# Performance work log

Hardware: AMD Instinct MI355X
Metric: run time of the kernel (lower is better)

## Reference

```python
import jax, jax.numpy as jnp
import numpy as np
import math

B, T, D, H = 4, 2048, 1024, 16
DH = D // H


def setup_inputs() -> dict:
    key = jax.random.key(0)
    k1, k2, k3 = jax.random.split(key, 3)
    x = jax.random.normal(k1, (B, T, D), dtype=jnp.float32)
    # causal mask: True = masked (positions j > i)
    attn_mask = jnp.triu(jnp.ones((T, T), dtype=bool), k=1)
    key_padding_mask = jnp.zeros((B, T), dtype=bool)  # no padding
    W_qkv = jax.random.normal(k2, (D, 3 * D), dtype=jnp.float32) / math.sqrt(D)
    W_out = jax.random.normal(k3, (D, D), dtype=jnp.float32) / math.sqrt(D)
    return {"x": x, "W_qkv": W_qkv, "W_out": W_out,
            "attn_mask": attn_mask, "key_padding_mask": key_padding_mask}


def reference(x, W_qkv, W_out, attn_mask, key_padding_mask):
    # qkv projection (bias=False)
    qkv = x @ W_qkv                                   # [B,T,3D]
    q, k, v = jnp.split(qkv, 3, axis=-1)              # each [B,T,D]
    # reshape to heads: [B,H,T,DH]
    q = q.reshape(B, T, H, DH).transpose(0, 2, 1, 3)
    k = k.reshape(B, T, H, DH).transpose(0, 2, 1, 3)
    v = v.reshape(B, T, H, DH).transpose(0, 2, 1, 3)
    scale = 1.0 / math.sqrt(DH)
    scores = jnp.einsum('bhqd,bhkd->bhqk', q, k) * scale   # [B,H,T,T]
    neg_inf = jnp.float32(-jnp.inf)
    scores = jnp.where(attn_mask[None, None, :, :], neg_inf, scores)
    scores = jnp.where(key_padding_mask[:, None, None, :], neg_inf, scores)
    attn = jax.nn.softmax(scores, axis=-1)            # dropout p=0.0 -> identity
    out = jnp.einsum('bhqk,bhkd->bhqd', attn, v)      # [B,H,T,DH]
    out = out.transpose(0, 2, 1, 3).reshape(B, T, D)
    return out @ W_out
```

## Files before the change

### kernel.cpp

```cpp
#include <hip/hip_runtime.h>
#include <hip/hip_bf16.h>

#define Bsz 4
#define T 2048
#define D 1024
#define H 16
#define DH 64

typedef unsigned short u16;
typedef __attribute__((ext_vector_type(8))) __bf16 bf16x8;
typedef __attribute__((ext_vector_type(4))) float f32x4;

__device__ inline u16 f2bf(float f) {
  union { float f; unsigned u; } v; v.f = f;
  unsigned r = (v.u + 0x7FFFu + ((v.u >> 16) & 1u)) >> 16;
  return (u16)r;
}
__device__ inline unsigned pack_bf16(float a, float b) {
  union { float f; unsigned u; } A, B; A.f = a; B.f = b;
  unsigned au = A.u + 0x8000u, bu = B.u + 0x8000u;
  return __builtin_amdgcn_perm(bu, au, 0x07060302);
}

__device__ inline void gll16(const u16* g, u16* l) {
  __builtin_amdgcn_global_load_lds((const __attribute__((address_space(1))) void*)g,
                                   (__attribute__((address_space(3))) void*)l, 16, 0, 0);
}

__global__ __launch_bounds__(256) void convert_f32_bf16(const float* __restrict__ in,
                                                        u16* __restrict__ out, int n4) {
  int i = blockIdx.x * 256 + threadIdx.x;
  if (i < n4) {
    float4 v = reinterpret_cast<const float4*>(in)[i];
    ushort4 o;
    o.x = f2bf(v.x); o.y = f2bf(v.y); o.z = f2bf(v.z); o.w = f2bf(v.w);
    reinterpret_cast<ushort4*>(out)[i] = o;
  }
}

__global__ __launch_bounds__(256) void transpose_f32_bf16(const float* __restrict__ in,
                                                          u16* __restrict__ out, int K, int N) {
  __shared__ float tile[32][33];
  int tx = threadIdx.x & 31, ty = threadIdx.x >> 5;
  int n0 = blockIdx.x * 32, k0 = blockIdx.y * 32;
  #pragma unroll
  for (int i = 0; i < 4; ++i)
    tile[ty + i * 8][tx] = in[(size_t)(k0 + ty + i * 8) * N + n0 + tx];
  __syncthreads();
  #pragma unroll
  for (int i = 0; i < 4; ++i)
    out[(size_t)(n0 + ty + i * 8) * K + k0 + tx] = f2bf(tile[tx][ty + i * 8]);
}

template <int MODE>
__global__ __launch_bounds__(256) void gemm128(const u16* __restrict__ A, const u16* __restrict__ BT,
                                               float* __restrict__ C,
                                               u16* __restrict__ Qh, u16* __restrict__ Kh,
                                               u16* __restrict__ VTh, int M, int N, int K) {
  __shared__ u16 As[128][32];
  __shared__ u16 Bs[128][32];
  int tid = threadIdx.x;
  int m0 = blockIdx.y * 128, n0 = blockIdx.x * 128;
  int w = tid >> 6, lane = tid & 63;
  int llo = lane & 15, lhi = lane >> 4;
  int wm = (w >> 1) * 64, wn = (w & 1) * 64;

  f32x4 acc[4][4];
  #pragma unroll
  for (int i = 0; i < 4; ++i)
    #pragma unroll
    for (int j = 0; j < 4; ++j) acc[i][j] = (f32x4){0.f, 0.f, 0.f, 0.f};

  const u16* gA = A + (size_t)(m0 + w * 32 + (lane >> 2)) * K + (lane & 3) * 8;
  const u16* gB = BT + (size_t)(n0 + w * 32 + (lane >> 2)) * K + (lane & 3) * 8;

  for (int k0 = 0; k0 < K; k0 += 32) {
    gll16(gA + k0, &As[w * 32][0]);
    gll16(gA + (size_t)16 * K + k0, &As[w * 32 + 16][0]);
    gll16(gB + k0, &Bs[w * 32][0]);
    gll16(gB + (size_t)16 * K + k0, &Bs[w * 32 + 16][0]);
    __syncthreads();
    bf16x8 af[4], bfr[4];
    #pragma unroll
    for (int i = 0; i < 4; ++i)
      af[i] = *reinterpret_cast<const bf16x8*>(&As[wm + i * 16 + llo][lhi * 8]);
    #pragma unroll
    for (int j = 0; j < 4; ++j)
      bfr[j] = *reinterpret_cast<const bf16x8*>(&Bs[wn + j * 16 + llo][lhi * 8]);
    #pragma unroll
    for (int i = 0; i < 4; ++i)
      #pragma unroll
      for (int j = 0; j < 4; ++j)
        acc[i][j] = __builtin_amdgcn_mfma_f32_16x16x32_bf16(af[i], bfr[j], acc[i][j], 0, 0, 0);
    __syncthreads();
  }

  if (MODE == 0) {
    #pragma unroll
    for (int i = 0; i < 4; ++i)
      #pragma unroll
      for (int j = 0; j < 4; ++j) {
        int nl = n0 + wn + j * 16 + llo;
        #pragma unroll
        for (int r = 0; r < 4; ++r) {
          int ml = m0 + wm + i * 16 + lhi * 4 + r;
          C[(size_t)ml * N + nl] = acc[i][j][r];
        }
      }
  } else {
    int seg = n0 >> 10;
    #pragma unroll
    for (int i = 0; i < 4; ++i) {
      int mbase = m0 + wm + i * 16 + lhi * 4;
      int t0 = mbase & (T - 1);
      int b_ = mbase >> 11;
      #pragma unroll
      for (int j = 0; j < 4; ++j) {
        int nl = n0 + wn + j * 16 + llo;
        int h = (nl >> 6) & 15, d = nl & 63;
        int bh = b_ * H + h;
        if (seg == 0) {
          #pragma unroll
          for (int r = 0; r < 4; ++r)
            Qh[((size_t)bh * T + t0 + r) * DH + d] = f2bf(acc[i][j][r] * 0.125f);
        } else if (seg == 1) {
          #pragma unroll
          for (int r = 0; r < 4; ++r)
            Kh[((size_t)bh * T + t0 + r) * DH + d] = f2bf(acc[i][j][r]);
        } else {
          uint2 p;
          p.x = pack_bf16(acc[i][j][0], acc[i][j][1]);
          p.y = pack_bf16(acc[i][j][2], acc[i][j][3]);
          *reinterpret_cast<uint2*>(&VTh[((size_t)bh * DH + d) * T + t0]) = p;
        }
      }
    }
  }
}

__global__ __launch_bounds__(1024, 4) void attn_fwd(const u16* __restrict__ Qh, const u16* __restrict__ Kh,
                                                    const u16* __restrict__ VTh, u16* __restrict__ AO) {
  __shared__ u16 QP[16][16][72];
  __shared__ u16 Ks[64][72];
  __shared__ u16 Vs[64][72];
  int tid = threadIdx.x;
  int qp = blockIdx.x, bh = blockIdx.y;
  int w = tid >> 6, lane = tid & 63;
  int llo = lane & 15, lhi = lane >> 4;

  int qrow_s = tid >> 2, qc = tid & 3;
  int krow_s = tid >> 4, kc = tid & 15;
  const u16* kbase = Kh + ((size_t)bh * T + krow_s) * DH + kc * 4;
  const u16* vbase = VTh + ((size_t)bh * DH + krow_s) * T + kc * 4;
  int b = bh >> 4, h = bh & 15;

  #pragma unroll 1
  for (int half = 0; half < 2; ++half) {
    int qt = half ? (7 - qp) : qp;
    int q0 = qt * 256;

    bf16x8 aq[2];
    {
      const uint4* g = reinterpret_cast<const uint4*>(
          Qh + ((size_t)bh * T + q0 + qrow_s) * DH + qc * 16);
      uint4 a = g[0], bb = g[1];
      uint4* dst = reinterpret_cast<uint4*>(&QP[w][qrow_s & 15][qc * 16]);
      dst[0] = a; dst[1] = bb;
      #pragma unroll
      for (int ks = 0; ks < 2; ++ks)
        aq[ks] = *reinterpret_cast<const bf16x8*>(&QP[w][llo][ks * 32 + lhi * 8]);
    }

    f32x4 o[4];
    #pragma unroll
    for (int i = 0; i < 4; ++i) o[i] = (f32x4){0.f, 0.f, 0.f, 0.f};
    float l_run = 0.f;

    int nj = 4 * qt + 4;
    uint2 ka = *reinterpret_cast<const uint2*>(kbase);
    uint2 va = *reinterpret_cast<const uint2*>(vbase);

    #pragma unroll 1
    for (int j = 0; j < nj; ++j) {
      __syncthreads();
      *reinterpret_cast<uint2*>(&Ks[krow_s][kc * 4]) = ka;
      *reinterpret_cast<uint2*>(&Vs[krow_s][kc * 4]) = va;
      if (j + 1 < nj) {
        ka = *reinterpret_cast<const uint2*>(kbase + (size_t)(j + 1) * 64 * DH);
        va = *reinterpret_cast<const uint2*>(vbase + (j + 1) * 64);
      } else if (half == 0) {
        ka = *reinterpret_cast<const uint2*>(kbase);
        va = *reinterpret_cast<const uint2*>(vbase);
      }
      __syncthreads();

      if (q0 + w * 16 + 15 >= j * 64) {
        f32x4 sc[4];
        #pragma unroll
        for (int kt = 0; kt < 4; ++kt) {
          bf16x8 bk0 = *reinterpret_cast<const bf16x8*>(&Ks[kt * 16 + llo][lhi * 8]);
          bf16x8 bk1 = *reinterpret_cast<const bf16x8*>(&Ks[kt * 16 + llo][32 + lhi * 8]);
          f32x4 z = (f32x4){0.f, 0.f, 0.f, 0.f};
          f32x4 t0 = __builtin_amdgcn_mfma_f32_16x16x32_bf16(bk0, aq[0], z, 0, 0, 0);
          sc[kt] = __builtin_amdgcn_mfma_f32_16x16x32_bf16(bk1, aq[1], t0, 0, 0, 0);
        }

        if (j >= 4 * qt) {
          int qrow_g = q0 + w * 16 + llo;
          #pragma unroll
          for (int kt = 0; kt < 4; ++kt)
            #pragma unroll
            for (int r = 0; r < 4; ++r) {
              int key_g = j * 64 + kt * 16 + lhi * 4 + r;
              if (key_g > qrow_g) sc[kt][r] = -__builtin_inff();
            }
        }

        float s_sum = 0.f;
        #pragma unroll
        for (int kt = 0; kt < 4; ++kt)
          #pragma unroll
          for (int r = 0; r < 4; ++r) {
            float p = __expf(sc[kt][r]);
            sc[kt][r] = p;
            s_sum += p;
          }
        s_sum += __shfl_xor(s_sum, 16);
        s_sum += __shfl_xor(s_sum, 32);
        l_run += s_sum;

        #pragma unroll
        for (int kt = 0; kt < 4; ++kt) {
          uint2 p;
          p.x = pack_bf16(sc[kt][0], sc[kt][1]);
          p.y = pack_bf16(sc[kt][2], sc[kt][3]);
          *reinterpret_cast<uint2*>(&QP[w][llo][kt * 16 + lhi * 4]) = p;
        }

        #pragma unroll
        for (int kk2 = 0; kk2 < 2; ++kk2) {
          bf16x8 pa = *reinterpret_cast<const bf16x8*>(&QP[w][llo][kk2 * 32 + lhi * 8]);
          #pragma unroll
          for (int nt = 0; nt < 4; ++nt) {
            bf16x8 bv = *reinterpret_cast<const bf16x8*>(&Vs[nt * 16 + llo][kk2 * 32 + lhi * 8]);
            o[nt] = __builtin_amdgcn_mfma_f32_16x16x32_bf16(pa, bv, o[nt], 0, 0, 0);
          }
        }
      }
    }

    #pragma unroll
    for (int r = 0; r < 4; ++r) {
      float inv = 1.f / __shfl(l_run, lhi * 4 + r);
      int t = q0 + w * 16 + lhi * 4 + r;
      #pragma unroll
      for (int nt = 0; nt < 4; ++nt)
        AO[((size_t)(b * T + t)) * D + h * 64 + nt * 16 + llo] = f2bf(o[nt][r] * inv);
    }
  }
}

extern "C" void kernel_launch(void* const* d_in, const int* in_sizes, int n_in,
                              void* d_out, int out_size, void* d_ws, size_t ws_size,
                              hipStream_t stream) {
  (void)in_sizes; (void)n_in; (void)out_size;
  const float* x = (const float*)d_in[0];
  const float* Wqkv = (const float*)d_in[1];
  const float* Wout = (const float*)d_in[2];
  float* out = (float*)d_out;

  char* ws = (char*)d_ws;
  size_t off = 0;
  u16* xb = (u16*)(ws + off);    off += (size_t)Bsz * T * D * 2;
  u16* WqkvT = (u16*)(ws + off); off += (size_t)3 * D * D * 2;
  u16* WoutT = (u16*)(ws + off); off += (size_t)D * D * 2;
  u16* Qh = (u16*)(ws + off);    off += (size_t)Bsz * H * T * DH * 2;
  u16* Kh = (u16*)(ws + off);    off += (size_t)Bsz * H * T * DH * 2;
  u16* VTh = (u16*)(ws + off);   off += (size_t)Bsz * H * DH * T * 2;
  u16* AO = xb;
  if (ws_size < off) return;

  int n4 = Bsz * T * D / 4;
  convert_f32_bf16<<<(n4 + 255) / 256, 256, 0, stream>>>(x, xb, n4);
  transpose_f32_bf16<<<dim3(3 * D / 32, D / 32), 256, 0, stream>>>(Wqkv, WqkvT, D, 3 * D);
  transpose_f32_bf16<<<dim3(D / 32, D / 32), 256, 0, stream>>>(Wout, WoutT, D, D);
  gemm128<1><<<dim3(3 * D / 128, Bsz * T / 128), 256, 0, stream>>>(xb, WqkvT, nullptr, Qh, Kh, VTh,
                                                                   Bsz * T, 3 * D, D);
  attn_fwd<<<dim3(4, Bsz * H), 1024, 0, stream>>>(Qh, Kh, VTh, AO);
  gemm128<0><<<dim3(D / 128, Bsz * T / 128), 256, 0, stream>>>(AO, WoutT, out, nullptr, nullptr, nullptr,
                                                               Bsz * T, D, D);
}
```

Measured before the change: 281.7 us.

## Replace QKV GEMM with 256x256 tiled, 4-stage pipelined kernel

```diff
diff --git a/kernel.cpp b/kernel.cpp
--- a/kernel.cpp
+++ b/kernel.cpp
@@ -50,6 +50,138 @@
   #pragma unroll
   for (int i = 0; i < 4; ++i)
     out[(size_t)(n0 + ty + i * 8) * K + k0 + tx] = f2bf(tile[tx][ty + i * 8]);
+}
+
+template <int MODE>
+__global__ __launch_bounds__(512, 2) void gemm256(const u16* __restrict__ A, const u16* __restrict__ BT,
+                                                  float* __restrict__ C,
+                                                  u16* __restrict__ Qh, u16* __restrict__ Kh,
+                                                  u16* __restrict__ VTh, int M, int N, int K) {
+  __shared__ alignas(16) u16 SA[4][8192];
+  __shared__ alignas(16) u16 SB[4][8192];
+  int tid = threadIdx.x;
+  int m0 = blockIdx.y * 256, n0 = blockIdx.x * 256;
+  int w = tid >> 6, lane = tid & 63;
+  int llo = lane & 15, lhi = lane >> 4;
+  int wr = w >> 2, wc = w & 3;
+  int swz = ((lhi ^ ((llo >> 1) & 3)) << 3);
+  int arow = (wr * 128 + llo) * 32;
+  int brow = (wc * 64 + llo) * 32;
+
+  int srcCol = (((tid & 3) ^ ((tid >> 3) & 3)) << 3);
+  const u16* gA0 = A + (size_t)(m0 + (tid >> 2)) * K + srcCol;
+  const u16* gA1 = gA0 + (size_t)128 * K;
+  const u16* gB0 = BT + (size_t)(n0 + (tid >> 2)) * K + srcCol;
+  const u16* gB1 = gB0 + (size_t)128 * K;
+
+  f32x4 acc[8][4];
+  #pragma unroll
+  for (int i = 0; i < 8; ++i)
+    #pragma unroll
+    for (int j = 0; j < 4; ++j) acc[i][j] = (f32x4){0.f, 0.f, 0.f, 0.f};
+
+  int nt = K >> 5;
+
+  #pragma unroll
+  for (int p = 0; p < 3; ++p) {
+    gll16(gA0 + p * 32, &SA[p][w * 512]);
+    gll16(gA1 + p * 32, &SA[p][4096 + w * 512]);
+    gll16(gB0 + p * 32, &SB[p][w * 512]);
+    gll16(gB1 + p * 32, &SB[p][4096 + w * 512]);
+  }
+  asm volatile("s_waitcnt vmcnt(8)" ::: "memory");
+  __builtin_amdgcn_s_barrier();
+
+  #pragma unroll 4
+  for (int t = 0; t < nt; ++t) {
+    int buf = t & 3;
+    const u16* sa = SA[buf];
+    const u16* sb = SB[buf];
+
+    bf16x8 af[8];
+    #pragma unroll
+    for (int i = 0; i < 8; ++i)
+      af[i] = *reinterpret_cast<const bf16x8*>(&sa[arow + i * 512 + swz]);
+    bf16x8 b0 = *reinterpret_cast<const bf16x8*>(&sb[brow + swz]);
+    bf16x8 b1 = *reinterpret_cast<const bf16x8*>(&sb[brow + 512 + swz]);
+    if (t + 3 < nt) {
+      gll16(gA0 + (t + 3) * 32, &SA[(t + 3) & 3][w * 512]);
+      gll16(gA1 + (t + 3) * 32, &SA[(t + 3) & 3][4096 + w * 512]);
+    }
+    __builtin_amdgcn_s_barrier();
+    asm volatile("s_waitcnt lgkmcnt(0)" ::: "memory");
+    __builtin_amdgcn_s_setprio(1);
+    #pragma unroll
+    for (int i = 0; i < 8; ++i) {
+      acc[i][0] = __builtin_amdgcn_mfma_f32_16x16x32_bf16(af[i], b0, acc[i][0], 0, 0, 0);
+      acc[i][1] = __builtin_amdgcn_mfma_f32_16x16x32_bf16(af[i], b1, acc[i][1], 0, 0, 0);
+    }
+    __builtin_amdgcn_s_setprio(0);
+    __builtin_amdgcn_s_barrier();
+
+    bf16x8 b2 = *reinterpret_cast<const bf16x8*>(&sb[brow + 1024 + swz]);
+    bf16x8 b3 = *reinterpret_cast<const bf16x8*>(&sb[brow + 1536 + swz]);
+    if (t + 3 < nt) {
+      gll16(gB0 + (t + 3) * 32, &SB[(t + 3) & 3][w * 512]);
+      gll16(gB1 + (t + 3) * 32, &SB[(t + 3) & 3][4096 + w * 512]);
+    }
+    __builtin_amdgcn_s_barrier();
+    asm volatile("s_waitcnt lgkmcnt(0)" ::: "memory");
+    __builtin_amdgcn_s_setprio(1);
+    #pragma unroll
+    for (int i = 0; i < 8; ++i) {
+      acc[i][2] = __builtin_amdgcn_mfma_f32_16x16x32_bf16(af[i], b2, acc[i][2], 0, 0, 0);
+      acc[i][3] = __builtin_amdgcn_mfma_f32_16x16x32_bf16(af[i], b3, acc[i][3], 0, 0, 0);
+    }
+    __builtin_amdgcn_s_setprio(0);
+    if (t + 3 < nt)      asm volatile("s_waitcnt vmcnt(8)" ::: "memory");
+    else if (t + 2 < nt) asm volatile("s_waitcnt vmcnt(4)" ::: "memory");
+    else if (t + 1 < nt) asm volatile("s_waitcnt vmcnt(0)" ::: "memory");
+    __builtin_amdgcn_s_barrier();
+    __builtin_amdgcn_sched_barrier(0);
+  }
+
+  if (MODE == 0) {
+    #pragma unroll
+    for (int i = 0; i < 8; ++i) {
+      int ml = m0 + wr * 128 + i * 16 + lhi * 4;
+      #pragma unroll
+      for (int j = 0; j < 4; ++j) {
+        int nl = n0 + wc * 64 + j * 16 + llo;
+        #pragma unroll
+        for (int r = 0; r < 4; ++r)
+          C[(size_t)(ml + r) * N + nl] = acc[i][j][r];
+      }
+    }
+  } else {
+    int seg = n0 >> 10;
+    #pragma unroll
+    for (int i = 0; i < 8; ++i) {
+      int mbase = m0 + wr * 128 + i * 16 + lhi * 4;
+      int t0 = mbase & (T - 1);
+      int b_ = mbase >> 11;
+      #pragma unroll
+      for (int j = 0; j < 4; ++j) {
+        int nl = n0 + wc * 64 + j * 16 + llo;
+        int h = (nl >> 6) & 15, d = nl & 63;
+        int bh = b_ * H + h;
+        if (seg == 0) {
+          #pragma unroll
+          for (int r = 0; r < 4; ++r)
+            Qh[((size_t)bh * T + t0 + r) * DH + d] = f2bf(acc[i][j][r] * 0.125f);
+        } else if (seg == 1) {
+          #pragma unroll
+          for (int r = 0; r < 4; ++r)
+            Kh[((size_t)bh * T + t0 + r) * DH + d] = f2bf(acc[i][j][r]);
+        } else {
+          uint2 p;
+          p.x = pack_bf16(acc[i][j][0], acc[i][j][1]);
+          p.y = pack_bf16(acc[i][j][2], acc[i][j][3]);
+          *reinterpret_cast<uint2*>(&VTh[((size_t)bh * DH + d) * T + t0]) = p;
+        }
+      }
+    }
+  }
 }
 
 template <int MODE>
@@ -107,34 +239,6 @@
           C[(size_t)ml * N + nl] = acc[i][j][r];
         }
       }
-  } else {
-    int seg = n0 >> 10;
-    #pragma unroll
-    for (int i = 0; i < 4; ++i) {
-      int mbase = m0 + wm + i * 16 + lhi * 4;
-      int t0 = mbase & (T - 1);
-      int b_ = mbase >> 11;
-      #pragma unroll
-      for (int j = 0; j < 4; ++j) {
-        int nl = n0 + wn + j * 16 + llo;
-        int h = (nl >> 6) & 15, d = nl & 63;
-        int bh = b_ * H + h;
-        if (seg == 0) {
-          #pragma unroll
-          for (int r = 0; r < 4; ++r)
-            Qh[((size_t)bh * T + t0 + r) * DH + d] = f2bf(acc[i][j][r] * 0.125f);
-        } else if (seg == 1) {
-          #pragma unroll
-          for (int r = 0; r < 4; ++r)
-            Kh[((size_t)bh * T + t0 + r) * DH + d] = f2bf(acc[i][j][r]);
-        } else {
-          uint2 p;
-          p.x = pack_bf16(acc[i][j][0], acc[i][j][1]);
-          p.y = pack_bf16(acc[i][j][2], acc[i][j][3]);
-          *reinterpret_cast<uint2*>(&VTh[((size_t)bh * DH + d) * T + t0]) = p;
-        }
-      }
-    }
   }
 }
 
@@ -284,7 +388,7 @@
   convert_f32_bf16<<<(n4 + 255) / 256, 256, 0, stream>>>(x, xb, n4);
   transpose_f32_bf16<<<dim3(3 * D / 32, D / 32), 256, 0, stream>>>(Wqkv, WqkvT, D, 3 * D);
   transpose_f32_bf16<<<dim3(D / 32, D / 32), 256, 0, stream>>>(Wout, WoutT, D, D);
-  gemm128<1><<<dim3(3 * D / 128, Bsz * T / 128), 256, 0, stream>>>(xb, WqkvT, nullptr, Qh, Kh, VTh,
+  gemm256<1><<<dim3(3 * D / 256, Bsz * T / 256), 512, 0, stream>>>(xb, WqkvT, nullptr, Qh, Kh, VTh,
                                                                    Bsz * T, 3 * D, D);
   attn_fwd<<<dim3(4, Bsz * H), 1024, 0, stream>>>(Qh, Kh, VTh, AO);
   gemm128<0><<<dim3(D / 128, Bsz * T / 128), 256, 0, stream>>>(AO, WoutT, out, nullptr, nullptr, nullptr,
```

Result: no change. 286.2 us (+1.6%).
